# Optimization experiments

Hardware: AMD Instinct MI355X
Metric: run time of the kernel (lower is better)

The kernel has to match this reference:

```python
import jax, jax.numpy as jnp
import numpy as np

N = 100000   # nodes
D = 64       # padded neighbor-list width (avg degree)
F = 256      # in_channels
H = 256      # hidden_channels
E = 131072   # number of target edges
OUT = 1      # out_channels


def _linear_params(key, fin, fout):
    k1, k2 = jax.random.split(key)
    s = 1.0 / np.sqrt(fin)
    w = jax.random.uniform(k1, (fin, fout), jnp.float32, -s, s)
    b = jax.random.uniform(k2, (fout,), jnp.float32, -s, s)
    return w, b


def setup_inputs() -> dict:
    key = jax.random.key(0)
    ks = jax.random.split(key, 12)
    x = jax.random.normal(ks[0], (N, F), jnp.float32)
    # sorted padded neighbor lists: row i -> D neighbor ids (sorted, as in the
    # bit-packed sorted-element representation the torch code intersects)
    neighbors = jnp.sort(jax.random.randint(ks[1], (N, D), 0, N), axis=1).astype(jnp.int32)
    tar_ei = jax.random.randint(ks[2], (2, E), 0, N).astype(jnp.int32)
    cn_w1, cn_b1 = _linear_params(ks[3], 1, H)
    cn_w2, cn_b2 = _linear_params(ks[4], H, H)
    cn_w3, cn_b3 = _linear_params(ks[5], H, H)
    ij_w1, ij_b1 = _linear_params(ks[6], F, H)
    ij_w2, ij_b2 = _linear_params(ks[7], H, H)
    lin_w1, lin_b1 = _linear_params(ks[8], H, H)
    lin_w2, lin_b2 = _linear_params(ks[9], H, OUT)
    beta = jnp.ones((1,), jnp.float32)
    return dict(x=x, neighbors=neighbors, tar_ei=tar_ei, beta=beta,
                cn_w1=cn_w1, cn_b1=cn_b1, cn_w2=cn_w2, cn_b2=cn_b2,
                cn_w3=cn_w3, cn_b3=cn_b3,
                ij_w1=ij_w1, ij_b1=ij_b1, ij_w2=ij_w2, ij_b2=ij_b2,
                lin_w1=lin_w1, lin_b1=lin_b1, lin_w2=lin_w2, lin_b2=lin_b2)


def reference(x, neighbors, tar_ei, beta,
              cn_w1, cn_b1, cn_w2, cn_b2, cn_w3, cn_b3,
              ij_w1, ij_b1, ij_w2, ij_b2,
              lin_w1, lin_b1, lin_w2, lin_b2):
    src, dst = tar_ei[0], tar_ei[1]
    xi = x[src]                       # [E, F] irregular gather
    xj = x[dst]                       # [E, F]

    # adjoverlap / spmoverlap_: per edge, |N(i) ∩ N(j)| via sorted-set
    # intersection; cn.sum(dim=-1) with fill value 1.0 -> CN count.
    ni = neighbors[src]               # [E, D]
    nj = neighbors[dst]               # [E, D]
    matches = ni[:, :, None] == nj[:, None, :]          # [E, D, D]
    xcn = jnp.sum(matches, axis=(1, 2)).astype(jnp.float32)[:, None]  # [E, 1]

    # xcnlin: Linear(1,H) -> ReLU -> Linear(H,H) -> ReLU -> Linear(H,H)
    h = jax.nn.relu(xcn @ cn_w1 + cn_b1)
    h = jax.nn.relu(h @ cn_w2 + cn_b2)
    xcn_feat = h @ cn_w3 + cn_b3                         # [E, H]

    # xijlin: Linear(F,H) -> ReLU -> Linear(H,H)
    g = jax.nn.relu((xi * xj) @ ij_w1 + ij_b1)
    xij = g @ ij_w2 + ij_b2                              # [E, H]

    # lin: Linear(H,H) -> ReLU -> Linear(H,OUT)
    z = jax.nn.relu((xcn_feat * beta + xij) @ lin_w1 + lin_b1)
    out = z @ lin_w2 + lin_b2                            # [E, OUT]
    return out
```

## Files before the change

kernel.cpp:

```cpp
#include <hip/hip_runtime.h>
#include <hip/hip_bf16.h>
#include <stdint.h>

#define EE 131072
#define DDEG 64

typedef __bf16 bf16_t;
typedef bf16_t bf16x8 __attribute__((ext_vector_type(8)));
typedef float floatx4 __attribute__((ext_vector_type(4)));

#define SWZ(row, k) (((row) << 8) + ((k) ^ (((row) & 7) << 3)))

__global__ __launch_bounds__(256)
void prep_kernel(const float* __restrict__ x, bf16_t* __restrict__ xb,
                 const float* __restrict__ ij_w1, bf16_t* __restrict__ Wt1,
                 const float* __restrict__ w2, const float* __restrict__ lw1,
                 bf16_t* __restrict__ Mt,
                 const float* __restrict__ b2, const float* __restrict__ lb1,
                 float* __restrict__ cvec,
                 const float* __restrict__ cw1, const float* __restrict__ cb1,
                 const float* __restrict__ cw2, const float* __restrict__ cb2,
                 const float* __restrict__ cw3, const float* __restrict__ cb3,
                 const float* __restrict__ beta, float* __restrict__ T2) {
    __shared__ __align__(16) char arena[33792];
    const int bid = blockIdx.x;
    const int t = threadIdx.x;

    if (bid >= 1088) {
        size_t base = (size_t)(bid - 1088) * 4096 + (size_t)t * 16;
        float4 a0 = *(const float4*)(x + base);
        float4 a1 = *(const float4*)(x + base + 4);
        float4 a2 = *(const float4*)(x + base + 8);
        float4 a3 = *(const float4*)(x + base + 12);
        bf16x8 o0, o1;
        o0[0] = (bf16_t)a0.x; o0[1] = (bf16_t)a0.y; o0[2] = (bf16_t)a0.z; o0[3] = (bf16_t)a0.w;
        o0[4] = (bf16_t)a1.x; o0[5] = (bf16_t)a1.y; o0[6] = (bf16_t)a1.z; o0[7] = (bf16_t)a1.w;
        o1[0] = (bf16_t)a2.x; o1[1] = (bf16_t)a2.y; o1[2] = (bf16_t)a2.z; o1[3] = (bf16_t)a2.w;
        o1[4] = (bf16_t)a3.x; o1[5] = (bf16_t)a3.y; o1[6] = (bf16_t)a3.z; o1[7] = (bf16_t)a3.w;
        *(bf16x8*)(xb + base)     = o0;
        *(bf16x8*)(xb + base + 8) = o1;
        return;
    }

    if (bid < 64) {
        float (*tile)[33] = (float (*)[33])arena;
        int bx = bid & 7, by = bid >> 3;
        int tx = t & 31, ty = t >> 5;
        #pragma unroll
        for (int r = 0; r < 32; r += 8)
            tile[ty + r][tx] = ij_w1[(by * 32 + ty + r) * 256 + bx * 32 + tx];
        __syncthreads();
        #pragma unroll
        for (int r = 0; r < 32; r += 8)
            Wt1[(bx * 32 + ty + r) * 256 + by * 32 + tx] = (bf16_t)tile[tx][ty + r];
    } else if (bid < 320) {
        float (*S)[33] = (float (*)[33])arena;
        int b = bid - 64;
        int cc = t & 31, abase = t >> 5;
        float acc = 0.f;
        for (int c0 = 0; c0 < 256; c0 += 32) {
            __syncthreads();
            #pragma unroll
            for (int r = 0; r < 32; ++r) {
                int a = r * 8 + abase;
                S[a][cc] = w2[a * 256 + c0 + cc];
            }
            __syncthreads();
            #pragma unroll 8
            for (int c2 = 0; c2 < 32; ++c2) {
                float wv = lw1[(c0 + c2) * 256 + b];
                acc += S[t][c2] * wv;
            }
        }
        Mt[(size_t)b * 256 + t] = (bf16_t)acc;
    } else if (bid < 576) {
        float* red = (float*)arena;
        int b = bid - 320;
        red[t] = b2[t] * lw1[t * 256 + b];
        __syncthreads();
        for (int s = 128; s > 0; s >>= 1) {
            if (t < s) red[t] += red[t + s];
            __syncthreads();
        }
        if (t == 0) cvec[b] = red[0] + lb1[b];
    } else {
        float* t1 = (float*)arena;
        float* t2 = (float*)(arena + 1024);
        float* t3 = (float*)(arena + 2048);
        int v = bid - 576;
        float fv = (float)v;
        t1[t] = fmaxf(fv * cw1[t] + cb1[t], 0.f);
        __syncthreads();
        float s = cb2[t];
        for (int k = 0; k < 256; ++k) s += t1[k] * cw2[k * 256 + t];
        t2[t] = fmaxf(s, 0.f);
        __syncthreads();
        s = cb3[t];
        for (int k = 0; k < 256; ++k) s += t2[k] * cw3[k * 256 + t];
        t3[t] = s * beta[0];
        __syncthreads();
        s = 0.f;
        for (int k = 0; k < 256; ++k) s += t3[k] * lw1[k * 256 + t];
        T2[(size_t)v * 256 + t] = s;
    }
}

__global__ __launch_bounds__(256, 3)
void fused_kernel(const bf16_t* __restrict__ xb, const int* __restrict__ tar,
                  const int* __restrict__ nbr,
                  const bf16_t* __restrict__ Wt1, const float* __restrict__ b1,
                  const bf16_t* __restrict__ Mt, const float* __restrict__ cvec,
                  const float* __restrict__ T2, int* __restrict__ xcnbuf,
                  const float* __restrict__ w2, const float* __restrict__ b2s,
                  float* __restrict__ out) {
    __shared__ __align__(16) bf16_t X[64 * 256];

    const int tid  = threadIdx.x;
    const int lane = tid & 63;
    const int wc   = tid >> 6;
    const int quad = lane >> 4;
    const int l16  = lane & 15;
    const int e0   = blockIdx.x * 64;

    {
        const int srow   = tid >> 2;
        const int skbase = (tid & 3) * 8;
        int e = e0 + srow;
        const bf16_t* xi = xb + (size_t)tar[e] * 256 + skbase;
        const bf16_t* xj = xb + (size_t)tar[EE + e] * 256 + skbase;
        bf16x8 ui[8], vj[8];
        #pragma unroll
        for (int kc = 0; kc < 8; ++kc) {
            ui[kc] = *(const bf16x8*)(xi + kc * 32);
            vj[kc] = *(const bf16x8*)(xj + kc * 32);
        }
        #pragma unroll
        for (int kc = 0; kc < 8; ++kc) {
            bf16x8 p;
            #pragma unroll
            for (int m = 0; m < 8; ++m)
                p[m] = (bf16_t)((float)ui[kc][m] * (float)vj[kc][m]);
            *(bf16x8*)&X[SWZ(srow, kc * 32 + skbase)] = p;
        }
    }

    __builtin_amdgcn_sched_barrier(0);

    int va[16], vb[16];
    #pragma unroll
    for (int i = 0; i < 16; ++i) {
        int e = e0 + wc * 16 + i;
        int s = __builtin_amdgcn_readfirstlane(tar[e]);
        int d = __builtin_amdgcn_readfirstlane(tar[EE + e]);
        va[i] = nbr[(size_t)s * DDEG + lane];
        vb[i] = nbr[(size_t)d * DDEG + lane];
    }

    __syncthreads();

    #pragma unroll
    for (int p = 0; p < 8; ++p) {
        int cpk = 0;
        #pragma unroll
        for (int h = 0; h < 2; ++h) {
            int i = p * 2 + h;
            int lo = 0, hi = 0;
            #pragma unroll
            for (int st = 32; st; st >>= 1) {
                int bl = __shfl(vb[i], lo + st - 1, 64);
                int bh = __shfl(vb[i], hi + st - 1, 64);
                lo += (bl < va[i]) ? st : 0;
                hi += (bh <= va[i]) ? st : 0;
            }
            int b63 = __shfl(vb[i], 63, 64);
            lo += (b63 < va[i]) ? 1 : 0;
            hi += (b63 <= va[i]) ? 1 : 0;
            cpk += (hi - lo) << (16 * h);
        }
        #pragma unroll
        for (int off = 32; off; off >>= 1) cpk += __shfl_xor(cpk, off, 64);
        if (lane == 0) {
            int c0 = cpk & 0xffff, c1 = (int)((unsigned)cpk >> 16);
            xcnbuf[e0 + wc * 16 + p * 2]     = c0 < 511 ? c0 : 511;
            xcnbuf[e0 + wc * 16 + p * 2 + 1] = c1 < 511 ? c1 : 511;
        }
    }

    floatx4 acc[4][4];
    #pragma unroll
    for (int i = 0; i < 4; ++i)
        #pragma unroll
        for (int j = 0; j < 4; ++j)
            acc[i][j] = (floatx4){0.f, 0.f, 0.f, 0.f};

    #pragma unroll 2
    for (int kc = 0; kc < 8; ++kc) {
        const int k0 = kc * 32 + quad * 8;
        bf16x8 af[4], bfr[4];
        #pragma unroll
        for (int j = 0; j < 4; ++j)
            bfr[j] = *(const bf16x8*)(Wt1 + (size_t)(wc * 64 + j * 16 + l16) * 256 + k0);
        #pragma unroll
        for (int i = 0; i < 4; ++i)
            af[i] = *(const bf16x8*)(&X[SWZ(i * 16 + l16, k0)]);
        #pragma unroll
        for (int i = 0; i < 4; ++i)
            #pragma unroll
            for (int j = 0; j < 4; ++j)
                acc[i][j] = __builtin_amdgcn_mfma_f32_16x16x32_bf16(
                                af[i], bfr[j], acc[i][j], 0, 0, 0);
    }

    __syncthreads();

    #pragma unroll
    for (int j = 0; j < 4; ++j) {
        int col  = wc * 64 + j * 16 + l16;
        float bv = b1[col];
        #pragma unroll
        for (int i = 0; i < 4; ++i)
            #pragma unroll
            for (int r = 0; r < 4; ++r) {
                int row = i * 16 + quad * 4 + r;
                X[SWZ(row, col)] = (bf16_t)fmaxf(acc[i][j][r] + bv, 0.f);
            }
    }
    #pragma unroll
    for (int i = 0; i < 4; ++i)
        #pragma unroll
        for (int j = 0; j < 4; ++j)
            acc[i][j] = (floatx4){0.f, 0.f, 0.f, 0.f};

    __syncthreads();

    #pragma unroll 2
    for (int kc = 0; kc < 8; ++kc) {
        const int k0 = kc * 32 + quad * 8;
        bf16x8 af[4], bfr[4];
        #pragma unroll
        for (int j = 0; j < 4; ++j)
            bfr[j] = *(const bf16x8*)(Mt + (size_t)(wc * 64 + j * 16 + l16) * 256 + k0);
        #pragma unroll
        for (int i = 0; i < 4; ++i)
            af[i] = *(const bf16x8*)(&X[SWZ(i * 16 + l16, k0)]);
        #pragma unroll
        for (int i = 0; i < 4; ++i)
            #pragma unroll
            for (int j = 0; j < 4; ++j)
                acc[i][j] = __builtin_amdgcn_mfma_f32_16x16x32_bf16(
                                af[i], bfr[j], acc[i][j], 0, 0, 0);
    }

    int xv[16];
    #pragma unroll
    for (int i = 0; i < 4; ++i)
        #pragma unroll
        for (int r = 0; r < 4; ++r)
            xv[i * 4 + r] = xcnbuf[e0 + i * 16 + quad * 4 + r];

    float pr[16];
    #pragma unroll
    for (int t = 0; t < 16; ++t) pr[t] = 0.f;
    #pragma unroll
    for (int j = 0; j < 4; ++j) {
        int col  = wc * 64 + j * 16 + l16;
        float cv = cvec[col];
        float wv = w2[col];
        #pragma unroll
        for (int i = 0; i < 4; ++i)
            #pragma unroll
            for (int r = 0; r < 4; ++r) {
                float t2v = T2[(size_t)xv[i * 4 + r] * 256 + col];
                float v = fmaxf(acc[i][j][r] + cv + t2v, 0.f);
                pr[i * 4 + r] += v * wv;
            }
    }
    #pragma unroll
    for (int off = 1; off < 16; off <<= 1)
        #pragma unroll
        for (int t = 0; t < 16; ++t)
            pr[t] += __shfl_xor(pr[t], off, 64);

    __syncthreads();
    float* red = (float*)X;
    if (l16 == 0) {
        #pragma unroll
        for (int i = 0; i < 4; ++i)
            #pragma unroll
            for (int r = 0; r < 4; ++r)
                red[wc * 64 + i * 16 + quad * 4 + r] = pr[i * 4 + r];
    }
    __syncthreads();
    if (tid < 64)
        out[e0 + tid] = red[tid] + red[64 + tid] + red[128 + tid]
                      + red[192 + tid] + b2s[0];
}

extern "C" void kernel_launch(void* const* d_in, const int* in_sizes, int n_in,
                              void* d_out, int out_size, void* d_ws, size_t ws_size,
                              hipStream_t stream) {
    const float* x      = (const float*)d_in[0];
    const int*   nbr    = (const int*)  d_in[1];
    const int*   tar    = (const int*)  d_in[2];
    const float* beta   = (const float*)d_in[3];
    const float* cn_w1  = (const float*)d_in[4];
    const float* cn_b1  = (const float*)d_in[5];
    const float* cn_w2  = (const float*)d_in[6];
    const float* cn_b2  = (const float*)d_in[7];
    const float* cn_w3  = (const float*)d_in[8];
    const float* cn_b3  = (const float*)d_in[9];
    const float* ij_w1  = (const float*)d_in[10];
    const float* ij_b1  = (const float*)d_in[11];
    const float* ij_w2  = (const float*)d_in[12];
    const float* ij_b2  = (const float*)d_in[13];
    const float* lin_w1 = (const float*)d_in[14];
    const float* lin_b1 = (const float*)d_in[15];
    const float* lin_w2 = (const float*)d_in[16];
    const float* lin_b2 = (const float*)d_in[17];

    char* ws = (char*)d_ws;
    float*  T2     = (float*) (ws + 0);
    int*    xcnbuf = (int*)   (ws + 524288);
    bf16_t* Wt1    = (bf16_t*)(ws + 1048576);
    bf16_t* Mt     = (bf16_t*)(ws + 1179648);
    float*  cvec   = (float*) (ws + 1310720);
    bf16_t* xb     = (bf16_t*)(ws + 1312768);

    prep_kernel<<<1088 + 6250, 256, 0, stream>>>(
        x, xb, ij_w1, Wt1, ij_w2, lin_w1, Mt,
        ij_b2, lin_b1, cvec,
        cn_w1, cn_b1, cn_w2, cn_b2, cn_w3, cn_b3, beta, T2);
    fused_kernel<<<EE / 64, 256, 0, stream>>>(xb, tar, nbr, Wt1, ij_b1, Mt, cvec,
                                              T2, xcnbuf, lin_w2, lin_b2,
                                              (float*)d_out);
}
```

Baseline: 316.9 us.

## Move common-neighbor intersection from fused kernel into prep kernel

The per-edge sorted neighbor-list intersection (neighbor gathers plus shuffle binary search) moves out of the fused MLP kernel into 2048 new blocks of the prep kernel, where it runs alongside the weight preprocessing and the x-to-bf16 conversion. The fused kernel now only reads precomputed counts from xcnbuf. The aim is to shrink register pressure and latency in the MFMA kernel and to overlap the intersection with the prep work. The product gather is also split into two chunks to lower live registers. The cost is an extra global round trip for the counts and a larger prep launch.

After: 318.8 us. Within noise of the previous version (+0.6%).

```diff
diff --git a/kernel.cpp b/kernel.cpp
--- a/kernel.cpp
+++ b/kernel.cpp
@@ -13,6 +13,8 @@
 
 __global__ __launch_bounds__(256)
 void prep_kernel(const float* __restrict__ x, bf16_t* __restrict__ xb,
+                 const int* __restrict__ tar, const int* __restrict__ nbr,
+                 int* __restrict__ xcnbuf,
                  const float* __restrict__ ij_w1, bf16_t* __restrict__ Wt1,
                  const float* __restrict__ w2, const float* __restrict__ lw1,
                  bf16_t* __restrict__ Mt,
@@ -26,8 +28,8 @@
     const int bid = blockIdx.x;
     const int t = threadIdx.x;
 
-    if (bid >= 1088) {
-        size_t base = (size_t)(bid - 1088) * 4096 + (size_t)t * 16;
+    if (bid >= 3136) {
+        size_t base = (size_t)(bid - 3136) * 4096 + (size_t)t * 16;
         float4 a0 = *(const float4*)(x + base);
         float4 a1 = *(const float4*)(x + base + 4);
         float4 a2 = *(const float4*)(x + base + 8);
@@ -42,9 +44,53 @@
         return;
     }
 
-    if (bid < 64) {
+    if (bid < 2048) {
+        const int lane = t & 63;
+        const int wcn  = t >> 6;
+        const int e0   = bid * 64 + wcn * 16;
+        int va[16], vb[16];
+        #pragma unroll
+        for (int i = 0; i < 16; ++i) {
+            int e = e0 + i;
+            int s = __builtin_amdgcn_readfirstlane(tar[e]);
+            int d = __builtin_amdgcn_readfirstlane(tar[EE + e]);
+            va[i] = nbr[(size_t)s * DDEG + lane];
+            vb[i] = nbr[(size_t)d * DDEG + lane];
+        }
+        #pragma unroll
+        for (int p = 0; p < 8; ++p) {
+            int cpk = 0;
+            #pragma unroll
+            for (int h = 0; h < 2; ++h) {
+                int i = p * 2 + h;
+                int lo = 0, hi = 0;
+                #pragma unroll
+                for (int st = 32; st; st >>= 1) {
+                    int bl = __shfl(vb[i], lo + st - 1, 64);
+                    int bh = __shfl(vb[i], hi + st - 1, 64);
+                    lo += (bl < va[i]) ? st : 0;
+                    hi += (bh <= va[i]) ? st : 0;
+                }
+                int b63 = __shfl(vb[i], 63, 64);
+                lo += (b63 < va[i]) ? 1 : 0;
+                hi += (b63 <= va[i]) ? 1 : 0;
+                cpk += (hi - lo) << (16 * h);
+            }
+            #pragma unroll
+            for (int off = 32; off; off >>= 1) cpk += __shfl_xor(cpk, off, 64);
+            if (lane == 0) {
+                int c0 = cpk & 0xffff, c1 = (int)((unsigned)cpk >> 16);
+                xcnbuf[e0 + p * 2]     = c0 < 511 ? c0 : 511;
+                xcnbuf[e0 + p * 2 + 1] = c1 < 511 ? c1 : 511;
+            }
+        }
+        return;
+    }
+
+    const int b2id = bid - 2048;
+    if (b2id < 64) {
         float (*tile)[33] = (float (*)[33])arena;
-        int bx = bid & 7, by = bid >> 3;
+        int bx = b2id & 7, by = b2id >> 3;
         int tx = t & 31, ty = t >> 5;
         #pragma unroll
         for (int r = 0; r < 32; r += 8)
@@ -53,9 +99,9 @@
         #pragma unroll
         for (int r = 0; r < 32; r += 8)
             Wt1[(bx * 32 + ty + r) * 256 + by * 32 + tx] = (bf16_t)tile[tx][ty + r];
-    } else if (bid < 320) {
+    } else if (b2id < 320) {
         float (*S)[33] = (float (*)[33])arena;
-        int b = bid - 64;
+        int b = b2id - 64;
         int cc = t & 31, abase = t >> 5;
         float acc = 0.f;
         for (int c0 = 0; c0 < 256; c0 += 32) {
@@ -73,9 +119,9 @@
             }
         }
         Mt[(size_t)b * 256 + t] = (bf16_t)acc;
-    } else if (bid < 576) {
+    } else if (b2id < 576) {
         float* red = (float*)arena;
-        int b = bid - 320;
+        int b = b2id - 320;
         red[t] = b2[t] * lw1[t * 256 + b];
         __syncthreads();
         for (int s = 128; s > 0; s >>= 1) {
@@ -87,7 +133,7 @@
         float* t1 = (float*)arena;
         float* t2 = (float*)(arena + 1024);
         float* t3 = (float*)(arena + 2048);
-        int v = bid - 576;
+        int v = b2id - 576;
         float fv = (float)v;
         t1[t] = fmaxf(fv * cw1[t] + cb1[t], 0.f);
         __syncthreads();
@@ -107,10 +153,9 @@
 
 __global__ __launch_bounds__(256, 3)
 void fused_kernel(const bf16_t* __restrict__ xb, const int* __restrict__ tar,
-                  const int* __restrict__ nbr,
                   const bf16_t* __restrict__ Wt1, const float* __restrict__ b1,
                   const bf16_t* __restrict__ Mt, const float* __restrict__ cvec,
-                  const float* __restrict__ T2, int* __restrict__ xcnbuf,
+                  const float* __restrict__ T2, const int* __restrict__ xcnbuf,
                   const float* __restrict__ w2, const float* __restrict__ b2s,
                   float* __restrict__ out) {
     __shared__ __align__(16) bf16_t X[64 * 256];
@@ -128,61 +173,22 @@
         int e = e0 + srow;
         const bf16_t* xi = xb + (size_t)tar[e] * 256 + skbase;
         const bf16_t* xj = xb + (size_t)tar[EE + e] * 256 + skbase;
-        bf16x8 ui[8], vj[8];
-        #pragma unroll
-        for (int kc = 0; kc < 8; ++kc) {
-            ui[kc] = *(const bf16x8*)(xi + kc * 32);
-            vj[kc] = *(const bf16x8*)(xj + kc * 32);
-        }
-        #pragma unroll
-        for (int kc = 0; kc < 8; ++kc) {
-            bf16x8 p;
-            #pragma unroll
-            for (int m = 0; m < 8; ++m)
-                p[m] = (bf16_t)((float)ui[kc][m] * (float)vj[kc][m]);
-            *(bf16x8*)&X[SWZ(srow, kc * 32 + skbase)] = p;
-        }
-    }
-
-    __builtin_amdgcn_sched_barrier(0);
-
-    int va[16], vb[16];
-    #pragma unroll
-    for (int i = 0; i < 16; ++i) {
-        int e = e0 + wc * 16 + i;
-        int s = __builtin_amdgcn_readfirstlane(tar[e]);
-        int d = __builtin_amdgcn_readfirstlane(tar[EE + e]);
-        va[i] = nbr[(size_t)s * DDEG + lane];
-        vb[i] = nbr[(size_t)d * DDEG + lane];
-    }
-
-    __syncthreads();
-
-    #pragma unroll
-    for (int p = 0; p < 8; ++p) {
-        int cpk = 0;
-        #pragma unroll
-        for (int h = 0; h < 2; ++h) {
-            int i = p * 2 + h;
-            int lo = 0, hi = 0;
-            #pragma unroll
-            for (int st = 32; st; st >>= 1) {
-                int bl = __shfl(vb[i], lo + st - 1, 64);
-                int bh = __shfl(vb[i], hi + st - 1, 64);
-                lo += (bl < va[i]) ? st : 0;
-                hi += (bh <= va[i]) ? st : 0;
-            }
-            int b63 = __shfl(vb[i], 63, 64);
-            lo += (b63 < va[i]) ? 1 : 0;
-            hi += (b63 <= va[i]) ? 1 : 0;
-            cpk += (hi - lo) << (16 * h);
-        }
-        #pragma unroll
-        for (int off = 32; off; off >>= 1) cpk += __shfl_xor(cpk, off, 64);
-        if (lane == 0) {
-            int c0 = cpk & 0xffff, c1 = (int)((unsigned)cpk >> 16);
-            xcnbuf[e0 + wc * 16 + p * 2]     = c0 < 511 ? c0 : 511;
-            xcnbuf[e0 + wc * 16 + p * 2 + 1] = c1 < 511 ? c1 : 511;
+        #pragma unroll
+        for (int c = 0; c < 2; ++c) {
+            bf16x8 ui[4], vj[4];
+            #pragma unroll
+            for (int k2 = 0; k2 < 4; ++k2) {
+                ui[k2] = *(const bf16x8*)(xi + (c * 4 + k2) * 32);
+                vj[k2] = *(const bf16x8*)(xj + (c * 4 + k2) * 32);
+            }
+            #pragma unroll
+            for (int k2 = 0; k2 < 4; ++k2) {
+                bf16x8 p;
+                #pragma unroll
+                for (int m = 0; m < 8; ++m)
+                    p[m] = (bf16_t)((float)ui[k2][m] * (float)vj[k2][m]);
+                *(bf16x8*)&X[SWZ(srow, (c * 4 + k2) * 32 + skbase)] = p;
+            }
         }
     }
 
@@ -192,6 +198,8 @@
         #pragma unroll
         for (int j = 0; j < 4; ++j)
             acc[i][j] = (floatx4){0.f, 0.f, 0.f, 0.f};
+
+    __syncthreads();
 
     #pragma unroll 2
     for (int kc = 0; kc < 8; ++kc) {
@@ -326,11 +334,12 @@
     float*  cvec   = (float*) (ws + 1310720);
     bf16_t* xb     = (bf16_t*)(ws + 1312768);
 
-    prep_kernel<<<1088 + 6250, 256, 0, stream>>>(
-        x, xb, ij_w1, Wt1, ij_w2, lin_w1, Mt,
+    prep_kernel<<<3136 + 6250, 256, 0, stream>>>(
+        x, xb, tar, nbr, xcnbuf,
+        ij_w1, Wt1, ij_w2, lin_w1, Mt,
         ij_b2, lin_b1, cvec,
         cn_w1, cn_b1, cn_w2, cn_b2, cn_w3, cn_b3, beta, T2);
-    fused_kernel<<<EE / 64, 256, 0, stream>>>(xb, tar, nbr, Wt1, ij_b1, Mt, cvec,
+    fused_kernel<<<EE / 64, 256, 0, stream>>>(xb, tar, Wt1, ij_b1, Mt, cvec,
                                               T2, xcnbuf, lin_w2, lin_b2,
                                               (float*)d_out);
 }
```
